# Kernel tuning notes

Hardware: AMD Instinct MI355X
Metric: run time of the kernel (lower is better)

## Reference

```python
import jax, jax.numpy as jnp
import numpy as np

N = 100000   # nodes
E = 1600000  # edges
F = 64       # node_features == latent_channels
H = 128      # hidden_channels
G = 256      # graphs
L = 2        # n_layers


def setup_inputs() -> dict:
    key = jax.random.key(0)
    ks = jax.random.split(key, 20)
    x = jax.random.normal(ks[0], (N, F), dtype=jnp.float32)
    u = jax.random.normal(ks[1], (G, 2), dtype=jnp.float32)
    edge_index = jax.random.randint(ks[2], (2, E), 0, N, dtype=jnp.int32)
    # evenly assign nodes to graphs (sorted segment ids, no empty segments)
    batch = (jnp.arange(N, dtype=jnp.int32) * G // N).astype(jnp.int32)
    s = 0.05
    # per-layer edge-MLP params, stacked over layers: in = 2F-2 = 126
    W1 = jax.random.normal(ks[3], (L, 2 * F - 2, H), dtype=jnp.float32) * s
    b1 = jnp.zeros((L, H), dtype=jnp.float32)
    W2 = jax.random.normal(ks[4], (L, H, H), dtype=jnp.float32) * s
    b2 = jnp.zeros((L, H), dtype=jnp.float32)
    W3 = jax.random.normal(ks[5], (L, H, F), dtype=jnp.float32) * s
    b3 = jnp.zeros((L, F), dtype=jnp.float32)
    # readout head: in = 3*F + 2 = 194
    LW1 = jax.random.normal(ks[6], (3 * F + 2, F), dtype=jnp.float32) * s
    Lb1 = jnp.zeros((F,), dtype=jnp.float32)
    LW2 = jax.random.normal(ks[7], (F, F), dtype=jnp.float32) * s
    Lb2 = jnp.zeros((F,), dtype=jnp.float32)
    LW3 = jax.random.normal(ks[8], (F, 2), dtype=jnp.float32) * s
    Lb3 = jnp.zeros((2,), dtype=jnp.float32)
    return dict(x=x, u=u, edge_index=edge_index, batch=batch,
                W1=W1, b1=b1, W2=W2, b2=b2, W3=W3, b3=b3,
                LW1=LW1, Lb1=Lb1, LW2=LW2, Lb2=Lb2, LW3=LW3, Lb3=Lb3)


def _edge_layer(x, src, dst, W1, b1, W2, b2, W3, b3):
    xi = x[dst]            # target nodes (x_i), [E, F]
    xj = x[src]            # source nodes (x_j), [E, F]
    d = xj[:, :3] - xi[:, :3]
    dist2 = jnp.sum(d * d, axis=-1, keepdims=True)  # [E, 1]
    m_in = jnp.concatenate([xi, xj[:, 3:], dist2], axis=-1)  # [E, 2F-2]
    h = jax.nn.silu(m_in @ W1 + b1)
    h = jax.nn.silu(h @ W2 + b2)
    m = jax.nn.silu(h @ W3 + b3)                    # [E, F]
    return jax.ops.segment_sum(m, dst, num_segments=N)  # aggr='sum'


def reference(x, u, edge_index, batch, W1, b1, W2, b2, W3, b3,
              LW1, Lb1, LW2, Lb2, LW3, Lb3):
    src, dst = edge_index[0], edge_index[1]
    for l in range(L):
        x = _edge_layer(x, src, dst, W1[l], b1[l], W2[l], b2[l], W3[l], b3[l])
    addp = jax.ops.segment_sum(x, batch, num_segments=G)
    cnt = jax.ops.segment_sum(jnp.ones((N, 1), x.dtype), batch, num_segments=G)
    meanp = addp / jnp.maximum(cnt, 1.0)
    maxp = jax.ops.segment_max(x, batch, num_segments=G)
    pooled = jnp.concatenate([addp, meanp, maxp, u], axis=1)  # [G, 3F+2]
    h = jax.nn.silu(pooled @ LW1 + Lb1)
    h = jax.nn.silu(h @ LW2 + Lb2)
    return h @ LW3 + Lb3  # [G, 2]
```

## Files before the change

### kernel.cpp

```cpp
#include <hip/hip_runtime.h>
#include <hip/hip_bf16.h>

typedef _Float16 f16;
typedef _Float16 f16x8 __attribute__((ext_vector_type(8)));
typedef float    f32x4 __attribute__((ext_vector_type(4)));
typedef float    f32x8 __attribute__((ext_vector_type(8)));

__device__ __forceinline__ float silu_f(float x) {
    return x * __builtin_amdgcn_rcpf(1.0f + __expf(-x));
}

__device__ __forceinline__ void load_lds16(const f16* g, f16* l) {
    __builtin_amdgcn_global_load_lds(
        (const __attribute__((address_space(1))) void*)g,
        (__attribute__((address_space(3))) void*)l, 16, 0, 0);
}

__global__ void prep_kernel(const float* __restrict__ W1, const float* __restrict__ W2,
                            const float* __restrict__ W3, f16* __restrict__ B1T,
                            f16* __restrict__ W2T, f16* __restrict__ W3T,
                            f16* __restrict__ w1c, int L, int total) {
    int idx = blockIdx.x * 256 + threadIdx.x;
    if (idx >= total) return;
    const int per = 16384 + 16384 + 8192 + 128;
    int l = idx / per, r = idx % per;
    const float* W1l = W1 + (size_t)l * 126 * 128;
    if (r < 16384) {
        int c = r >> 6, k = r & 63;
        float v;
        if (c < 128) v = W1l[k * 128 + c];
        else v = (k >= 3) ? W1l[(64 + k - 3) * 128 + (c - 128)]
                          : 0.0f;
        B1T[(size_t)l * 16384 + r] = (f16)v;
    } else if (r < 32768) {
        int q = r - 16384, n = q >> 7, k = q & 127;
        W2T[(size_t)l * 16384 + q] = (f16)W2[(size_t)l * 16384 + k * 128 + n];
    } else if (r < 40960) {
        int q = r - 32768, n = q >> 7, k = q & 127;
        W3T[(size_t)l * 8192 + q] = (f16)W3[(size_t)l * 8192 + k * 64 + n];
    } else {
        int c = r - 40960;
        w1c[l * 128 + c] = (f16)W1l[125 * 128 + c];
    }
}

__global__ void hist_kernel(const int* __restrict__ ei, int* __restrict__ deg, int E) {
    int i = blockIdx.x * 256 + threadIdx.x;
    if (i < E) atomicAdd(&deg[ei[E + i]], 1);
}

__global__ void scan_part(const int* __restrict__ deg, int* __restrict__ bsum, int N) {
    __shared__ int red[256];
    int t = threadIdx.x;
    int i = blockIdx.x * 256 + t;
    red[t] = (i < N) ? deg[i] : 0;
    __syncthreads();
    for (int s = 128; s > 0; s >>= 1) {
        if (t < s) red[t] += red[t + s];
        __syncthreads();
    }
    if (t == 0) bsum[blockIdx.x] = red[0];
}

__global__ void scan_mid(const int* __restrict__ bsum, int* __restrict__ boff, int nb) {
    __shared__ int sm[512];
    int t = threadIdx.x;
    int v = (t < nb) ? bsum[t] : 0;
    sm[t] = v;
    __syncthreads();
    for (int off = 1; off < 512; off <<= 1) {
        int a = (t >= off) ? sm[t - off] : 0;
        __syncthreads();
        sm[t] += a;
        __syncthreads();
    }
    if (t < nb) boff[t] = sm[t] - v;
}

__global__ void scan_final(const int* __restrict__ deg, const int* __restrict__ boff,
                           int* __restrict__ row_start, int N) {
    __shared__ int sm[256];
    int t = threadIdx.x;
    int i = blockIdx.x * 256 + t;
    int v = (i < N) ? deg[i] : 0;
    sm[t] = v;
    __syncthreads();
    for (int off = 1; off < 256; off <<= 1) {
        int a = (t >= off) ? sm[t - off] : 0;
        __syncthreads();
        sm[t] += a;
        __syncthreads();
    }
    if (i < N) row_start[i] = boff[blockIdx.x] + sm[t] - v;
}

__global__ void scatter_kernel(const int* __restrict__ ei, const int* __restrict__ row_start,
                               int* __restrict__ cursor, int* __restrict__ srcs,
                               int* __restrict__ dsts, int E) {
    int i = blockIdx.x * 256 + threadIdx.x;
    if (i < E) {
        int d = ei[E + i];
        int p = row_start[d] + atomicAdd(&cursor[d], 1);
        srcs[p] = ei[i];
        dsts[p] = d;
    }
}

__global__ __launch_bounds__(256, 3) void node_kernel(
    const float* __restrict__ x, const f16* __restrict__ B1T,
    const float* __restrict__ b1, f16* __restrict__ PQ,
    float4* __restrict__ C, int N, int ntiles) {
    __shared__ f16 b1t[256 * 72];
    const int tid = threadIdx.x;
    const int w = tid >> 6, lane = tid & 63, lm = lane & 15, kg = lane >> 4;

    for (int i = tid; i < 256 * 64; i += 256)
        b1t[(i >> 6) * 72 + (i & 63)] = B1T[i];
    __syncthreads();

    for (int tile = blockIdx.x; tile < ntiles; tile += gridDim.x) {
        const int base = tile * 64;
        int ar = base + w * 16 + lm;
        if (ar >= N) ar = N - 1;

        f16x8 afrag[2];
#pragma unroll
        for (int ks = 0; ks < 2; ks++) {
            f32x8 v = *(const f32x8*)(x + (size_t)ar * 64 + ks * 32 + kg * 8);
            f16x8 h;
#pragma unroll
            for (int j = 0; j < 8; j++) h[j] = (f16)v[j];
            afrag[ks] = h;
        }

        f32x4 acc[16];
#pragma unroll
        for (int nb = 0; nb < 16; nb++) acc[nb] = (f32x4){0.f, 0.f, 0.f, 0.f};
#pragma unroll
        for (int ks = 0; ks < 2; ks++)
#pragma unroll
            for (int nb = 0; nb < 16; nb++) {
                f16x8 b = *(const f16x8*)&b1t[(nb * 16 + lm) * 72 + ks * 32 + kg * 8];
                acc[nb] = __builtin_amdgcn_mfma_f32_16x16x32_f16(afrag[ks], b, acc[nb], 0, 0, 0);
            }

#pragma unroll
        for (int nb = 0; nb < 16; nb++) {
            int col = nb * 16 + lm;
            float bias = (col < 128) ? b1[col] : 0.0f;
#pragma unroll
            for (int reg = 0; reg < 4; reg++) {
                int orow = base + w * 16 + kg * 4 + reg;
                if (orow < N) PQ[(size_t)orow * 256 + col] = (f16)(acc[nb][reg] + bias);
            }
        }
        if (tid < 64) {
            int n = base + tid;
            if (n < N) {
                const float* xr = x + (size_t)n * 64;
                C[n] = make_float4(xr[0], xr[1], xr[2], 0.0f);
            }
        }
    }
}

__global__ __launch_bounds__(256, 2) void edge_kernel(
    const f16* __restrict__ PQ, const float4* __restrict__ C,
    const int* __restrict__ srcs, const int* __restrict__ dsts,
    const f16* __restrict__ W2T, const f16* __restrict__ W3T,
    const f16* __restrict__ w1c, const float* __restrict__ b2,
    const float* __restrict__ b3, float* __restrict__ xout,
    int E, int wtiles) {
    __shared__ f16 w2t[128 * 128];
    __shared__ f16 stage[4 * 4096];
    __shared__ f16 tb[4 * 16 * 72];

    const int tid = threadIdx.x;
    const int w = tid >> 6, lane = tid & 63, lm = lane & 15, kg = lane >> 4;
    const int e4 = lane >> 2, c4 = lane & 3;

    for (int i = tid; i < 128 * 128; i += 256) {
        int n = i >> 7, k = i & 127;
        w2t[n * 128 + (((k >> 3) ^ (n & 15)) << 3) + (k & 7)] = W2T[i];
    }

    f32x8 wvh[4];
#pragma unroll
    for (int ks = 0; ks < 4; ks++) {
        f16x8 wv = *(const f16x8*)(w1c + ks * 32 + kg * 8);
#pragma unroll
        for (int j = 0; j < 8; j++) wvh[ks][j] = (float)wv[j];
    }
    float bias2[8], bias3[4];
#pragma unroll
    for (int nb = 0; nb < 8; nb++) bias2[nb] = b2[nb * 16 + lm];
#pragma unroll
    for (int nb = 0; nb < 4; nb++) bias3[nb] = b3[nb * 16 + lm];
    __syncthreads();

    f16* sw = stage + w * 4096;
    f16* tq = tb + w * (16 * 72);
    const int nwaves = gridDim.x * 4;
    const int r0 = kg * 4;
    const int l1i = (lane + 16) & 63, l2i = (lane + 32) & 63, l3i = (lane + 48) & 63;

    int t = blockIdx.x * 4 + w;
    if (t >= wtiles) return;
    int e0 = t * 16 + lm;
    int erc = min(e0, E - 1);
    int scl = srcs[erc];
    int dcl = dsts[erc];
    int dsen_cur = (e0 < E) ? dcl : -1;
    {
        int de = __shfl(dcl, e4), se = __shfl(scl, e4);
        const f16* gp = PQ + (size_t)de * 256 + c4 * 8;
        const f16* gq = PQ + (size_t)se * 256 + 128 + c4 * 8;
#pragma unroll
        for (int j = 0; j < 4; j++) load_lds16(gp + j * 32, sw + j * 512 + lane * 8);
#pragma unroll
        for (int j = 0; j < 4; j++) load_lds16(gq + j * 32, sw + 2048 + j * 512 + lane * 8);
    }
    int e1 = (t + nwaves) * 16 + lm;
    int erc1 = min(max(e1, 0), E - 1);
    int s_nx = srcs[erc1];
    int d_nx = dsts[erc1];
    int e_nx_ok = (e1 < E) ? 1 : 0;
    float4 cs = C[scl], cd = C[dcl];

    f32x4 acc2p[4];
#pragma unroll
    for (int nb2 = 0; nb2 < 4; nb2++) acc2p[nb2] = (f32x4){0.f, 0.f, 0.f, 0.f};
    int dsen_prev = -1;

    while (true) {
        const int tn = t + nwaves;

        asm volatile("s_waitcnt vmcnt(4)" ::: "memory");

        float dx = cs.x - cd.x, dy = cs.y - cd.y, dz = cs.z - cd.z;
        float dist2 = dx * dx + dy * dy + dz * dz;

        f16x8 afrag[4];
#pragma unroll
        for (int ks = 0; ks < 4; ks++) {
            f16x8 p = *(const f16x8*)&sw[ks * 512 + lm * 32 + kg * 8];
            f16x8 q = *(const f16x8*)&sw[2048 + ks * 512 + lm * 32 + kg * 8];
            f16x8 pq = p + q;
            f16x8 h;
#pragma unroll
            for (int j = 0; j < 8; j++) {
                float v = (float)pq[j] + dist2 * wvh[ks][j];
                h[j] = (f16)silu_f(v);
            }
            afrag[ks] = h;
        }

        f32x4 acc1[8];
#pragma unroll
        for (int nb = 0; nb < 8; nb++) acc1[nb] = (f32x4){0.f, 0.f, 0.f, 0.f};
#pragma unroll
        for (int ks = 0; ks < 4; ks++)
#pragma unroll
            for (int nb = 0; nb < 8; nb++) {
                int n = nb * 16 + lm;
                f16x8 b = *(const f16x8*)&w2t[n * 128 + (((ks * 4 + kg) ^ (n & 15)) << 3)];
                acc1[nb] = __builtin_amdgcn_mfma_f32_16x16x32_f16(afrag[ks], b, acc1[nb], 0, 0, 0);
            }

        {
            const int dr0 = __shfl(dsen_prev, r0);
            const int dr1 = __shfl(dsen_prev, r0 + 1);
            const int dr2 = __shfl(dsen_prev, r0 + 2);
            const int dr3 = __shfl(dsen_prev, r0 + 3);
            int prevv = __shfl(dsen_prev, (r0 - 1) & 63);
            if (kg == 0) prevv = -1234567;

            const bool e01 = dr0 == dr1, e12 = dr1 == dr2, e23 = dr2 == dr3;
            const bool c01 = e01, c02 = e01 && e12, c03 = c02 && e23;
            const bool c12 = e12, c13 = e12 && e23;
            const int fullI = c03 ? 1 : 0;

            const int tgt = dr3;
            const int dr0_1 = __shfl(dr0, l1i), fu1 = __shfl(fullI, l1i);
            const int dr0_2 = __shfl(dr0, l2i), fu2 = __shfl(fullI, l2i);
            const int dr0_3 = __shfl(dr0, l3i);
            const bool take1 = (kg <= 2) && (dr0_1 == tgt);
            const bool take2 = take1 && fu1 && (kg <= 1) && (dr0_2 == tgt);
            const bool take3 = take2 && fu2 && (kg == 0) && (dr0_3 == tgt);

            const bool h0 = (dr0 != prevv) && (dr0 >= 0);
            const bool h1f = (!e01) && (dr1 >= 0);
            const bool h2f = (!e12) && (dr2 >= 0);
            const bool h3f = (!e23) && (dr3 >= 0);

            float t0v[4], t1v[4], t2v[4], t3v[4];
#pragma unroll
            for (int nb2 = 0; nb2 < 4; nb2++) {
                const float bias = bias3[nb2];
                const float v0 = silu_f(acc2p[nb2][0] + bias);
                const float v1 = silu_f(acc2p[nb2][1] + bias);
                const float v2 = silu_f(acc2p[nb2][2] + bias);
                const float v3 = silu_f(acc2p[nb2][3] + bias);
                float lead = v0 + (c01 ? v1 : 0.f) + (c02 ? v2 : 0.f) + (c03 ? v3 : 0.f);
                float ext = 0.f;
                const float le1 = __shfl(lead, l1i);
                const float le2 = __shfl(lead, l2i);
                const float le3 = __shfl(lead, l3i);
                if (take1) ext += le1;
                if (take2) ext += le2;
                if (take3) ext += le3;
                t0v[nb2] = lead + (c03 ? ext : 0.f);
                t1v[nb2] = v1 + (c12 ? v2 : 0.f) + (c13 ? (v3 + ext) : 0.f);
                t2v[nb2] = v2 + (e23 ? (v3 + ext) : 0.f);
                t3v[nb2] = v3 + ext;
            }
            if (h0) {
                float* p = xout + (size_t)dr0 * 64 + lm;
#pragma unroll
                for (int nb2 = 0; nb2 < 4; nb2++) atomicAdd(p + nb2 * 16, t0v[nb2]);
            }
            if (h1f) {
                float* p = xout + (size_t)dr1 * 64 + lm;
#pragma unroll
                for (int nb2 = 0; nb2 < 4; nb2++) atomicAdd(p + nb2 * 16, t1v[nb2]);
            }
            if (h2f) {
                float* p = xout + (size_t)dr2 * 64 + lm;
#pragma unroll
                for (int nb2 = 0; nb2 < 4; nb2++) atomicAdd(p + nb2 * 16, t2v[nb2]);
            }
            if (h3f) {
                float* p = xout + (size_t)dr3 * 64 + lm;
#pragma unroll
                for (int nb2 = 0; nb2 < 4; nb2++) atomicAdd(p + nb2 * 16, t3v[nb2]);
            }
        }

        int dsen_nx = e_nx_ok ? d_nx : -1;
        if (tn < wtiles) {
            int de = __shfl(d_nx, e4), se = __shfl(s_nx, e4);
            const f16* gp = PQ + (size_t)de * 256 + c4 * 8;
            const f16* gq = PQ + (size_t)se * 256 + 128 + c4 * 8;
#pragma unroll
            for (int j = 0; j < 4; j++) load_lds16(gp + j * 32, sw + j * 512 + lane * 8);
#pragma unroll
            for (int j = 0; j < 4; j++) load_lds16(gq + j * 32, sw + 2048 + j * 512 + lane * 8);
        }

        int e2 = (tn + nwaves) * 16 + lm;
        int erc2 = min(max(e2, 0), E - 1);
        int s_nx2 = srcs[erc2];
        int d_nx2 = dsts[erc2];
        int e_nx2_ok = (e2 < E) ? 1 : 0;
        float4 cs2 = C[s_nx], cd2 = C[d_nx];

        f32x4 acc2[4];
#pragma unroll
        for (int nb2 = 0; nb2 < 4; nb2++) acc2[nb2] = (f32x4){0.f, 0.f, 0.f, 0.f};
#pragma unroll
        for (int half = 0; half < 2; half++) {
#pragma unroll
            for (int kqi = 0; kqi < 2; kqi++) {
                int kq = half * 2 + kqi;
#pragma unroll
                for (int nn = 0; nn < 2; nn++) {
                    int nb = kq * 2 + nn;
#pragma unroll
                    for (int reg = 0; reg < 4; reg++)
                        tq[(kg * 4 + reg) * 72 + kqi * 32 + nn * 16 + lm] =
                            (f16)silu_f(acc1[nb][reg] + bias2[nb]);
                }
            }
#pragma unroll
            for (int kqi = 0; kqi < 2; kqi++) {
                int kq = half * 2 + kqi;
                f16x8 a2 = *(const f16x8*)&tq[lm * 72 + kqi * 32 + kg * 8];
#pragma unroll
                for (int nb2 = 0; nb2 < 4; nb2++) {
                    f16x8 b = *(const f16x8*)(W3T + (size_t)(nb2 * 16 + lm) * 128 +
                                              kq * 32 + kg * 8);
                    acc2[nb2] = __builtin_amdgcn_mfma_f32_16x16x32_f16(a2, b, acc2[nb2], 0, 0, 0);
                }
            }
        }

#pragma unroll
        for (int nb2 = 0; nb2 < 4; nb2++) acc2p[nb2] = acc2[nb2];
        dsen_prev = dsen_cur;
        dsen_cur = dsen_nx;
        s_nx = s_nx2; d_nx = d_nx2; e_nx_ok = e_nx2_ok;
        cs = cs2; cd = cd2;
        t = tn;
        if (t >= wtiles) break;
    }

    {
        const int dr0 = __shfl(dsen_prev, r0);
        const int dr1 = __shfl(dsen_prev, r0 + 1);
        const int dr2 = __shfl(dsen_prev, r0 + 2);
        const int dr3 = __shfl(dsen_prev, r0 + 3);
        int prevv = __shfl(dsen_prev, (r0 - 1) & 63);
        if (kg == 0) prevv = -1234567;

        const bool e01 = dr0 == dr1, e12 = dr1 == dr2, e23 = dr2 == dr3;
        const bool c01 = e01, c02 = e01 && e12, c03 = c02 && e23;
        const bool c12 = e12, c13 = e12 && e23;
        const int fullI = c03 ? 1 : 0;

        const int tgt = dr3;
        const int dr0_1 = __shfl(dr0, l1i), fu1 = __shfl(fullI, l1i);
        const int dr0_2 = __shfl(dr0, l2i), fu2 = __shfl(fullI, l2i);
        const int dr0_3 = __shfl(dr0, l3i);
        const bool take1 = (kg <= 2) && (dr0_1 == tgt);
        const bool take2 = take1 && fu1 && (kg <= 1) && (dr0_2 == tgt);
        const bool take3 = take2 && fu2 && (kg == 0) && (dr0_3 == tgt);

        const bool h0 = (dr0 != prevv) && (dr0 >= 0);
        const bool h1f = (!e01) && (dr1 >= 0);
        const bool h2f = (!e12) && (dr2 >= 0);
        const bool h3f = (!e23) && (dr3 >= 0);

        float t0v[4], t1v[4], t2v[4], t3v[4];
#pragma unroll
        for (int nb2 = 0; nb2 < 4; nb2++) {
            const float bias = bias3[nb2];
            const float v0 = silu_f(acc2p[nb2][0] + bias);
            const float v1 = silu_f(acc2p[nb2][1] + bias);
            const float v2 = silu_f(acc2p[nb2][2] + bias);
            const float v3 = silu_f(acc2p[nb2][3] + bias);
            float lead = v0 + (c01 ? v1 : 0.f) + (c02 ? v2 : 0.f) + (c03 ? v3 : 0.f);
            float ext = 0.f;
            const float le1 = __shfl(lead, l1i);
            const float le2 = __shfl(lead, l2i);
            const float le3 = __shfl(lead, l3i);
            if (take1) ext += le1;
            if (take2) ext += le2;
            if (take3) ext += le3;
            t0v[nb2] = lead + (c03 ? ext : 0.f);
            t1v[nb2] = v1 + (c12 ? v2 : 0.f) + (c13 ? (v3 + ext) : 0.f);
            t2v[nb2] = v2 + (e23 ? (v3 + ext) : 0.f);
            t3v[nb2] = v3 + ext;
        }
        if (h0) {
            float* p = xout + (size_t)dr0 * 64 + lm;
#pragma unroll
            for (int nb2 = 0; nb2 < 4; nb2++) atomicAdd(p + nb2 * 16, t0v[nb2]);
        }
        if (h1f) {
            float* p = xout + (size_t)dr1 * 64 + lm;
#pragma unroll
            for (int nb2 = 0; nb2 < 4; nb2++) atomicAdd(p + nb2 * 16, t1v[nb2]);
        }
        if (h2f) {
            float* p = xout + (size_t)dr2 * 64 + lm;
#pragma unroll
            for (int nb2 = 0; nb2 < 4; nb2++) atomicAdd(p + nb2 * 16, t2v[nb2]);
        }
        if (h3f) {
            float* p = xout + (size_t)dr3 * 64 + lm;
#pragma unroll
            for (int nb2 = 0; nb2 < 4; nb2++) atomicAdd(p + nb2 * 16, t3v[nb2]);
        }
    }
    asm volatile("s_waitcnt vmcnt(0)" ::: "memory");
}

__global__ void pool_kernel(const float* __restrict__ xf, const float* __restrict__ u,
                            float* __restrict__ pooled, int N, int G) {
    int g = blockIdx.x;
    int t = threadIdx.x;
    int ch = t & 63, sub = t >> 6;
    long long n0 = ((long long)g * N + G - 1) / G;
    long long n1 = ((long long)(g + 1) * N + G - 1) / G;
    float sm = 0.f, mx = -3.0e38f;
    for (long long n = n0 + sub; n < n1; n += 4) {
        float v = xf[n * 64 + ch];
        sm += v;
        mx = fmaxf(mx, v);
    }
    __shared__ float ssum[256], smax[256];
    ssum[t] = sm;
    smax[t] = mx;
    __syncthreads();
    if (sub == 0) {
        float a = ssum[ch] + ssum[64 + ch] + ssum[128 + ch] + ssum[192 + ch];
        float m = fmaxf(fmaxf(smax[ch], smax[64 + ch]), fmaxf(smax[128 + ch], smax[192 + ch]));
        float cnt = (float)(n1 - n0);
        pooled[g * 194 + ch] = a;
        pooled[g * 194 + 64 + ch] = a / fmaxf(cnt, 1.f);
        pooled[g * 194 + 128 + ch] = m;
    }
    if (t == 0) {
        pooled[g * 194 + 192] = u[g * 2];
        pooled[g * 194 + 193] = u[g * 2 + 1];
    }
}

__global__ void head_kernel(const float* __restrict__ pooled,
                            const float* __restrict__ LW1, const float* __restrict__ Lb1,
                            const float* __restrict__ LW2, const float* __restrict__ Lb2,
                            const float* __restrict__ LW3, const float* __restrict__ Lb3,
                            float* __restrict__ out, int G) {
    int g = blockIdx.x, t = threadIdx.x;
    __shared__ float pl[194];
    __shared__ float hl[64];
    for (int k = t; k < 194; k += 64) pl[k] = pooled[g * 194 + k];
    __syncthreads();
    float a = Lb1[t];
    for (int k = 0; k < 194; k++) a += pl[k] * LW1[k * 64 + t];
    a = a / (1.0f + __expf(-a));
    hl[t] = a;
    __syncthreads();
    float b = Lb2[t];
    for (int k = 0; k < 64; k++) b += hl[k] * LW2[k * 64 + t];
    b = b / (1.0f + __expf(-b));
    __syncthreads();
    hl[t] = b;
    __syncthreads();
    if (t < 2) {
        float c = Lb3[t];
        for (int k = 0; k < 64; k++) c += hl[k] * LW3[k * 2 + t];
        out[g * 2 + t] = c;
    }
}

extern "C" void kernel_launch(void* const* d_in, const int* in_sizes, int n_in,
                              void* d_out, int out_size, void* d_ws, size_t ws_size,
                              hipStream_t stream) {
    const float* x   = (const float*)d_in[0];
    const float* u   = (const float*)d_in[1];
    const int*   ei  = (const int*)d_in[2];
    const float* W1  = (const float*)d_in[4];
    const float* b1  = (const float*)d_in[5];
    const float* W2  = (const float*)d_in[6];
    const float* b2  = (const float*)d_in[7];
    const float* W3  = (const float*)d_in[8];
    const float* b3  = (const float*)d_in[9];
    const float* LW1 = (const float*)d_in[10];
    const float* Lb1 = (const float*)d_in[11];
    const float* LW2 = (const float*)d_in[12];
    const float* Lb2 = (const float*)d_in[13];
    const float* LW3 = (const float*)d_in[14];
    const float* Lb3 = (const float*)d_in[15];

    const int N = in_sizes[0] / 64;
    const int G = in_sizes[1] / 2;
    const int E = in_sizes[2] / 2;
    const int L = in_sizes[4] / (126 * 128);

    char* ws = (char*)d_ws;
    size_t off = 0;
    auto alloc = [&](size_t bytes) -> char* {
        char* p = ws + off;
        off += (bytes + 511) & ~(size_t)511;
        return p;
    };
    f16*    PQ     = (f16*)alloc((size_t)N * 256 * 2);
    float4* C      = (float4*)alloc((size_t)N * 16);
    float*  x1     = (float*)alloc((size_t)N * 64 * 4);
    float*  x2     = (float*)alloc((size_t)N * 64 * 4);
    int*    srcs   = (int*)alloc((size_t)E * 4);
    int*    dsts   = (int*)alloc((size_t)E * 4);
    int*    deg    = (int*)alloc((size_t)N * 4);
    int*    rowst  = (int*)alloc((size_t)N * 4);
    int*    cursor = (int*)alloc((size_t)N * 4);
    int*    bsum   = (int*)alloc(4096);
    int*    boff   = (int*)alloc(4096);
    f16*    B1T    = (f16*)alloc((size_t)L * 256 * 64 * 2);
    f16*    W2T    = (f16*)alloc((size_t)L * 128 * 128 * 2);
    f16*    W3T    = (f16*)alloc((size_t)L * 64 * 128 * 2);
    f16*    w1c    = (f16*)alloc((size_t)L * 128 * 2);
    float*  pooled = (float*)alloc((size_t)G * 194 * 4);
    (void)ws_size;
    (void)n_in;
    (void)out_size;

    hipMemsetAsync(deg, 0, (size_t)N * 4, stream);
    hipMemsetAsync(cursor, 0, (size_t)N * 4, stream);
    hipMemsetAsync(x1, 0, (size_t)N * 64 * 4, stream);
    hipMemsetAsync(x2, 0, (size_t)N * 64 * 4, stream);

    {
        int total = L * (16384 + 16384 + 8192 + 128);
        prep_kernel<<<(total + 255) / 256, 256, 0, stream>>>(W1, W2, W3, B1T, W2T, W3T, w1c, L, total);
    }
    hist_kernel<<<(E + 255) / 256, 256, 0, stream>>>(ei, deg, E);
    int NB = (N + 255) / 256;
    scan_part<<<NB, 256, 0, stream>>>(deg, bsum, N);
    scan_mid<<<1, 512, 0, stream>>>(bsum, boff, NB);
    scan_final<<<NB, 256, 0, stream>>>(deg, boff, rowst, N);
    scatter_kernel<<<(E + 255) / 256, 256, 0, stream>>>(ei, rowst, cursor, srcs, dsts, E);

    const float* xcur = x;
    const int wtiles = (E + 15) / 16;
    const int ntiles_node = (N + 63) / 64;
    for (int l = 0; l < L; l++) {
        node_kernel<<<768, 256, 0, stream>>>(xcur, B1T + (size_t)l * 16384, b1 + l * 128,
                                             PQ, C, N, ntiles_node);
        float* xo = (l & 1) ? x2 : x1;
        edge_kernel<<<512, 256, 0, stream>>>(PQ, C, srcs, dsts,
                                             W2T + (size_t)l * 16384, W3T + (size_t)l * 8192,
                                             w1c + l * 128, b2 + l * 128, b3 + l * 64,
                                             xo, E, wtiles);
        xcur = xo;
    }
    pool_kernel<<<G, 256, 0, stream>>>(xcur, u, pooled, N, G);
    head_kernel<<<G, 64, 0, stream>>>(pooled, LW1, Lb1, LW2, Lb2, LW3, Lb3, (float*)d_out, G);
}
```

Before: 1.035 ms.

## Use packed f16 SiLU, stage W3 in LDS, pack src/dst, fuse pool+head

The first-layer SiLU on edges now runs in packed half precision using v_exp_f16/v_rcp_f16, replacing the fp32 exp/rcp path. W3T is staged in swizzled LDS instead of being read from global memory in the inner loop. The per-tile transpose buffer shrinks to process one k-quarter at a time. Source and destination indices are interleaved as int2 so one load replaces two, which changes the vmcnt wait count. The pool and head kernels are merged into one launch, dropping the pooled buffer. The f16 activation loses accuracy, and the extra LDS may reduce occupancy.

```diff
diff --git a/kernel.cpp b/kernel.cpp
--- a/kernel.cpp
+++ b/kernel.cpp
@@ -8,6 +8,28 @@
 
 __device__ __forceinline__ float silu_f(float x) {
     return x * __builtin_amdgcn_rcpf(1.0f + __expf(-x));
+}
+
+__device__ __forceinline__ f16 exp2h(f16 x) {
+    short r, xs = __builtin_bit_cast(short, x);
+    asm("v_exp_f16 %0, %1" : "=v"(r) : "v"(xs));
+    return __builtin_bit_cast(f16, r);
+}
+__device__ __forceinline__ f16 rcph(f16 x) {
+    short r, xs = __builtin_bit_cast(short, x);
+    asm("v_rcp_f16 %0, %1" : "=v"(r) : "v"(xs));
+    return __builtin_bit_cast(f16, r);
+}
+__device__ __forceinline__ f16x8 silu_h8(f16x8 x) {
+    f16x8 t = x * (f16)(-1.442695040f);
+    f16x8 e;
+#pragma unroll
+    for (int j = 0; j < 8; j++) e[j] = exp2h(t[j]);
+    f16x8 d = e + (f16)1.0f;
+    f16x8 r;
+#pragma unroll
+    for (int j = 0; j < 8; j++) r[j] = rcph(d[j]);
+    return x * r;
 }
 
 __device__ __forceinline__ void load_lds16(const f16* g, f16* l) {
@@ -29,8 +51,7 @@
         int c = r >> 6, k = r & 63;
         float v;
         if (c < 128) v = W1l[k * 128 + c];
-        else v = (k >= 3) ? W1l[(64 + k - 3) * 128 + (c - 128)]
-                          : 0.0f;
+        else v = (k >= 3) ? W1l[(64 + k - 3) * 128 + (c - 128)] : 0.0f;
         B1T[(size_t)l * 16384 + r] = (f16)v;
     } else if (r < 32768) {
         int q = r - 16384, n = q >> 7, k = q & 127;
@@ -95,14 +116,12 @@
 }
 
 __global__ void scatter_kernel(const int* __restrict__ ei, const int* __restrict__ row_start,
-                               int* __restrict__ cursor, int* __restrict__ srcs,
-                               int* __restrict__ dsts, int E) {
+                               int* __restrict__ cursor, int2* __restrict__ sd, int E) {
     int i = blockIdx.x * 256 + threadIdx.x;
     if (i < E) {
         int d = ei[E + i];
         int p = row_start[d] + atomicAdd(&cursor[d], 1);
-        srcs[p] = ei[i];
-        dsts[p] = d;
+        sd[p] = make_int2(ei[i], d);
     }
 }
 
@@ -166,14 +185,15 @@
 
 __global__ __launch_bounds__(256, 2) void edge_kernel(
     const f16* __restrict__ PQ, const float4* __restrict__ C,
-    const int* __restrict__ srcs, const int* __restrict__ dsts,
+    const int2* __restrict__ sd,
     const f16* __restrict__ W2T, const f16* __restrict__ W3T,
     const f16* __restrict__ w1c, const float* __restrict__ b2,
     const float* __restrict__ b3, float* __restrict__ xout,
     int E, int wtiles) {
     __shared__ f16 w2t[128 * 128];
     __shared__ f16 stage[4 * 4096];
-    __shared__ f16 tb[4 * 16 * 72];
+    __shared__ f16 w3t[64 * 128];
+    __shared__ f16 tb[4 * 576];
 
     const int tid = threadIdx.x;
     const int w = tid >> 6, lane = tid & 63, lm = lane & 15, kg = lane >> 4;
@@ -183,14 +203,14 @@
         int n = i >> 7, k = i & 127;
         w2t[n * 128 + (((k >> 3) ^ (n & 15)) << 3) + (k & 7)] = W2T[i];
     }
-
-    f32x8 wvh[4];
-#pragma unroll
-    for (int ks = 0; ks < 4; ks++) {
-        f16x8 wv = *(const f16x8*)(w1c + ks * 32 + kg * 8);
-#pragma unroll
-        for (int j = 0; j < 8; j++) wvh[ks][j] = (float)wv[j];
-    }
+    for (int i = tid; i < 64 * 128; i += 256) {
+        int n = i >> 7, k = i & 127;
+        w3t[n * 128 + (((k >> 3) ^ (n & 15)) << 3) + (k & 7)] = W3T[i];
+    }
+
+    f16x8 wvh[4];
+#pragma unroll
+    for (int ks = 0; ks < 4; ks++) wvh[ks] = *(const f16x8*)(w1c + ks * 32 + kg * 8);
     float bias2[8], bias3[4];
 #pragma unroll
     for (int nb = 0; nb < 8; nb++) bias2[nb] = b2[nb * 16 + lm];
@@ -199,7 +219,7 @@
     __syncthreads();
 
     f16* sw = stage + w * 4096;
-    f16* tq = tb + w * (16 * 72);
+    f16* tq = tb + w * 576;
     const int nwaves = gridDim.x * 4;
     const int r0 = kg * 4;
     const int l1i = (lane + 16) & 63, l2i = (lane + 32) & 63, l3i = (lane + 48) & 63;
@@ -208,8 +228,8 @@
     if (t >= wtiles) return;
     int e0 = t * 16 + lm;
     int erc = min(e0, E - 1);
-    int scl = srcs[erc];
-    int dcl = dsts[erc];
+    int2 sd0 = sd[erc];
+    int scl = sd0.x, dcl = sd0.y;
     int dsen_cur = (e0 < E) ? dcl : -1;
     {
         int de = __shfl(dcl, e4), se = __shfl(scl, e4);
@@ -222,8 +242,8 @@
     }
     int e1 = (t + nwaves) * 16 + lm;
     int erc1 = min(max(e1, 0), E - 1);
-    int s_nx = srcs[erc1];
-    int d_nx = dsts[erc1];
+    int2 sdn = sd[erc1];
+    int s_nx = sdn.x, d_nx = sdn.y;
     int e_nx_ok = (e1 < E) ? 1 : 0;
     float4 cs = C[scl], cd = C[dcl];
 
@@ -235,24 +255,19 @@
     while (true) {
         const int tn = t + nwaves;
 
-        asm volatile("s_waitcnt vmcnt(4)" ::: "memory");
+        asm volatile("s_waitcnt vmcnt(3)" ::: "memory");
 
         float dx = cs.x - cd.x, dy = cs.y - cd.y, dz = cs.z - cd.z;
         float dist2 = dx * dx + dy * dy + dz * dz;
+        f16 d2h = (f16)dist2;
 
         f16x8 afrag[4];
 #pragma unroll
         for (int ks = 0; ks < 4; ks++) {
             f16x8 p = *(const f16x8*)&sw[ks * 512 + lm * 32 + kg * 8];
             f16x8 q = *(const f16x8*)&sw[2048 + ks * 512 + lm * 32 + kg * 8];
-            f16x8 pq = p + q;
-            f16x8 h;
-#pragma unroll
-            for (int j = 0; j < 8; j++) {
-                float v = (float)pq[j] + dist2 * wvh[ks][j];
-                h[j] = (f16)silu_f(v);
-            }
-            afrag[ks] = h;
+            f16x8 xv = p + q + d2h * wvh[ks];
+            afrag[ks] = silu_h8(xv);
         }
 
         f32x4 acc1[8];
@@ -349,8 +364,7 @@
 
         int e2 = (tn + nwaves) * 16 + lm;
         int erc2 = min(max(e2, 0), E - 1);
-        int s_nx2 = srcs[erc2];
-        int d_nx2 = dsts[erc2];
+        int2 sd2 = sd[erc2];
         int e_nx2_ok = (e2 < E) ? 1 : 0;
         float4 cs2 = C[s_nx], cd2 = C[d_nx];
 
@@ -358,29 +372,21 @@
 #pragma unroll
         for (int nb2 = 0; nb2 < 4; nb2++) acc2[nb2] = (f32x4){0.f, 0.f, 0.f, 0.f};
 #pragma unroll
-        for (int half = 0; half < 2; half++) {
-#pragma unroll
-            for (int kqi = 0; kqi < 2; kqi++) {
-                int kq = half * 2 + kqi;
-#pragma unroll
-                for (int nn = 0; nn < 2; nn++) {
-                    int nb = kq * 2 + nn;
-#pragma unroll
-                    for (int reg = 0; reg < 4; reg++)
-                        tq[(kg * 4 + reg) * 72 + kqi * 32 + nn * 16 + lm] =
-                            (f16)silu_f(acc1[nb][reg] + bias2[nb]);
-                }
-            }
-#pragma unroll
-            for (int kqi = 0; kqi < 2; kqi++) {
-                int kq = half * 2 + kqi;
-                f16x8 a2 = *(const f16x8*)&tq[lm * 72 + kqi * 32 + kg * 8];
-#pragma unroll
-                for (int nb2 = 0; nb2 < 4; nb2++) {
-                    f16x8 b = *(const f16x8*)(W3T + (size_t)(nb2 * 16 + lm) * 128 +
-                                              kq * 32 + kg * 8);
-                    acc2[nb2] = __builtin_amdgcn_mfma_f32_16x16x32_f16(a2, b, acc2[nb2], 0, 0, 0);
-                }
+        for (int kq = 0; kq < 4; kq++) {
+#pragma unroll
+            for (int nn = 0; nn < 2; nn++) {
+                int nb = kq * 2 + nn;
+#pragma unroll
+                for (int reg = 0; reg < 4; reg++)
+                    tq[(kg * 4 + reg) * 36 + nn * 16 + lm] =
+                        (f16)silu_f(acc1[nb][reg] + bias2[nb]);
+            }
+            f16x8 a2 = *(const f16x8*)&tq[lm * 36 + kg * 8];
+#pragma unroll
+            for (int nb2 = 0; nb2 < 4; nb2++) {
+                int n = nb2 * 16 + lm;
+                f16x8 b = *(const f16x8*)&w3t[n * 128 + (((kq * 4 + kg) ^ (n & 15)) << 3)];
+                acc2[nb2] = __builtin_amdgcn_mfma_f32_16x16x32_f16(a2, b, acc2[nb2], 0, 0, 0);
             }
         }
 
@@ -388,7 +394,7 @@
         for (int nb2 = 0; nb2 < 4; nb2++) acc2p[nb2] = acc2[nb2];
         dsen_prev = dsen_cur;
         dsen_cur = dsen_nx;
-        s_nx = s_nx2; d_nx = d_nx2; e_nx_ok = e_nx2_ok;
+        s_nx = sd2.x; d_nx = sd2.y; e_nx_ok = e_nx2_ok;
         cs = cs2; cd = cd2;
         t = tn;
         if (t >= wtiles) break;
@@ -465,8 +471,11 @@
     asm volatile("s_waitcnt vmcnt(0)" ::: "memory");
 }
 
-__global__ void pool_kernel(const float* __restrict__ xf, const float* __restrict__ u,
-                            float* __restrict__ pooled, int N, int G) {
+__global__ void pool_head_kernel(const float* __restrict__ xf, const float* __restrict__ u,
+                                 const float* __restrict__ LW1, const float* __restrict__ Lb1,
+                                 const float* __restrict__ LW2, const float* __restrict__ Lb2,
+                                 const float* __restrict__ LW3, const float* __restrict__ Lb3,
+                                 float* __restrict__ out, int N, int G) {
     int g = blockIdx.x;
     int t = threadIdx.x;
     int ch = t & 63, sub = t >> 6;
@@ -479,6 +488,8 @@
         mx = fmaxf(mx, v);
     }
     __shared__ float ssum[256], smax[256];
+    __shared__ float pl[194];
+    __shared__ float hl[64];
     ssum[t] = sm;
     smax[t] = mx;
     __syncthreads();
@@ -486,36 +497,31 @@
         float a = ssum[ch] + ssum[64 + ch] + ssum[128 + ch] + ssum[192 + ch];
         float m = fmaxf(fmaxf(smax[ch], smax[64 + ch]), fmaxf(smax[128 + ch], smax[192 + ch]));
         float cnt = (float)(n1 - n0);
-        pooled[g * 194 + ch] = a;
-        pooled[g * 194 + 64 + ch] = a / fmaxf(cnt, 1.f);
-        pooled[g * 194 + 128 + ch] = m;
+        pl[ch] = a;
+        pl[64 + ch] = a / fmaxf(cnt, 1.f);
+        pl[128 + ch] = m;
     }
     if (t == 0) {
-        pooled[g * 194 + 192] = u[g * 2];
-        pooled[g * 194 + 193] = u[g * 2 + 1];
-    }
-}
-
-__global__ void head_kernel(const float* __restrict__ pooled,
-                            const float* __restrict__ LW1, const float* __restrict__ Lb1,
-                            const float* __restrict__ LW2, const float* __restrict__ Lb2,
-                            const float* __restrict__ LW3, const float* __restrict__ Lb3,
-                            float* __restrict__ out, int G) {
-    int g = blockIdx.x, t = threadIdx.x;
-    __shared__ float pl[194];
-    __shared__ float hl[64];
-    for (int k = t; k < 194; k += 64) pl[k] = pooled[g * 194 + k];
-    __syncthreads();
-    float a = Lb1[t];
-    for (int k = 0; k < 194; k++) a += pl[k] * LW1[k * 64 + t];
-    a = a / (1.0f + __expf(-a));
-    hl[t] = a;
-    __syncthreads();
-    float b = Lb2[t];
-    for (int k = 0; k < 64; k++) b += hl[k] * LW2[k * 64 + t];
-    b = b / (1.0f + __expf(-b));
-    __syncthreads();
-    hl[t] = b;
+        pl[192] = u[g * 2];
+        pl[193] = u[g * 2 + 1];
+    }
+    __syncthreads();
+    float a = 0.f;
+    if (t < 64) {
+        a = Lb1[t];
+        for (int k = 0; k < 194; k++) a += pl[k] * LW1[k * 64 + t];
+        a = a / (1.0f + __expf(-a));
+        hl[t] = a;
+    }
+    __syncthreads();
+    float b = 0.f;
+    if (t < 64) {
+        b = Lb2[t];
+        for (int k = 0; k < 64; k++) b += hl[k] * LW2[k * 64 + t];
+        b = b / (1.0f + __expf(-b));
+    }
+    __syncthreads();
+    if (t < 64) hl[t] = b;
     __syncthreads();
     if (t < 2) {
         float c = Lb3[t];
@@ -559,8 +565,7 @@
     float4* C      = (float4*)alloc((size_t)N * 16);
     float*  x1     = (float*)alloc((size_t)N * 64 * 4);
     float*  x2     = (float*)alloc((size_t)N * 64 * 4);
-    int*    srcs   = (int*)alloc((size_t)E * 4);
-    int*    dsts   = (int*)alloc((size_t)E * 4);
+    int2*   sd     = (int2*)alloc((size_t)E * 8);
     int*    deg    = (int*)alloc((size_t)N * 4);
     int*    rowst  = (int*)alloc((size_t)N * 4);
     int*    cursor = (int*)alloc((size_t)N * 4);
@@ -570,7 +575,6 @@
     f16*    W2T    = (f16*)alloc((size_t)L * 128 * 128 * 2);
     f16*    W3T    = (f16*)alloc((size_t)L * 64 * 128 * 2);
     f16*    w1c    = (f16*)alloc((size_t)L * 128 * 2);
-    float*  pooled = (float*)alloc((size_t)G * 194 * 4);
     (void)ws_size;
     (void)n_in;
     (void)out_size;
@@ -589,7 +593,7 @@
     scan_part<<<NB, 256, 0, stream>>>(deg, bsum, N);
     scan_mid<<<1, 512, 0, stream>>>(bsum, boff, NB);
     scan_final<<<NB, 256, 0, stream>>>(deg, boff, rowst, N);
-    scatter_kernel<<<(E + 255) / 256, 256, 0, stream>>>(ei, rowst, cursor, srcs, dsts, E);
+    scatter_kernel<<<(E + 255) / 256, 256, 0, stream>>>(ei, rowst, cursor, sd, E);
 
     const float* xcur = x;
     const int wtiles = (E + 15) / 16;
@@ -598,12 +602,12 @@
         node_kernel<<<768, 256, 0, stream>>>(xcur, B1T + (size_t)l * 16384, b1 + l * 128,
                                              PQ, C, N, ntiles_node);
         float* xo = (l & 1) ? x2 : x1;
-        edge_kernel<<<512, 256, 0, stream>>>(PQ, C, srcs, dsts,
+        edge_kernel<<<512, 256, 0, stream>>>(PQ, C, sd,
                                              W2T + (size_t)l * 16384, W3T + (size_t)l * 8192,
                                              w1c + l * 128, b2 + l * 128, b3 + l * 64,
                                              xo, E, wtiles);
         xcur = xo;
     }
-    pool_kernel<<<G, 256, 0, stream>>>(xcur, u, pooled, N, G);
-    head_kernel<<<G, 64, 0, stream>>>(pooled, LW1, Lb1, LW2, Lb2, LW3, Lb3, (float*)d_out, G);
-}
+    pool_head_kernel<<<G, 256, 0, stream>>>(xcur, u, LW1, Lb1, LW2, Lb2, LW3, Lb3,
+                                            (float*)d_out, N, G);
+}
```

Result: slower. 1.133 ms (+9.5%).
